# Optimization experiments

Measured on AMD Instinct MI355X. Metric: run time of the kernel, lower is better.

The kernel has to match this reference:

```python
import jax, jax.numpy as jnp
import numpy as np

B, N, F, K = 512, 512, 512, 10
D = F // 2

def setup_inputs() -> dict:
    key = jax.random.key(0)
    k1, k2, k3 = jax.random.split(key, 3)
    ins_emb = jax.random.normal(k1, (B, N, F), dtype=jnp.float32)
    attn = jax.random.uniform(k2, (B, N, 1), dtype=jnp.float32)
    # xavier_uniform for a (D, D) linear weight
    limit = float(np.sqrt(6.0 / (D + D)))
    W = jax.random.uniform(k3, (D, D), dtype=jnp.float32, minval=-limit, maxval=limit)
    return {"ins_emb": ins_emb, "attn": attn, "W": W}

def reference(ins_emb, attn, W):
    d = ins_emb.shape[-1] // 2
    drug = ins_emb[:, :, :d]          # [B, N, d]
    dis = ins_emb[:, :, d:]           # [B, N, d]
    # torch Linear: drug @ W^T, then per-instance dot with dis -> scalar
    proj = jnp.einsum('bnd,ed->bne', drug, W)          # [B, N, d]
    pred = jnp.sum(proj * dis, axis=-1, keepdims=True) # [B, N, 1]
    attn_pred = attn * pred                            # [B, N, 1]
    topk_vals, _ = jax.lax.top_k(attn_pred[:, :, 0], K)  # [B, K]
    return jnp.mean(topk_vals, axis=1, keepdims=True)    # [B, 1]
```

## Files before the change

### kernel.cpp

```cpp
#include <hip/hip_runtime.h>
#include <hip/hip_bf16.h>
#include <cstdint>

#define BB 512
#define NN 512
#define FF 512
#define DD 256
#define KTOP 10
#define BN (BB*NN)
#define BM 32
#define NTILES (BN/BM)
#define GRID 256
#define TPB (NTILES/GRID)

typedef __attribute__((ext_vector_type(8))) short bf16x8;
typedef __attribute__((ext_vector_type(4))) short s16x4;
typedef __attribute__((ext_vector_type(4))) float f32x4;

__device__ __forceinline__ ushort f2bf(float x){
  union { __hip_bfloat16 h; ushort u; } cv;
  cv.h = __float2bfloat16(x);
  return cv.u;
}

__device__ __forceinline__ bf16x8 cvt8(f32x4 a, f32x4 b){
  bf16x8 r;
  r[0]=(short)f2bf(a[0]); r[1]=(short)f2bf(a[1]); r[2]=(short)f2bf(a[2]); r[3]=(short)f2bf(a[3]);
  r[4]=(short)f2bf(b[0]); r[5]=(short)f2bf(b[1]); r[6]=(short)f2bf(b[2]); r[7]=(short)f2bf(b[3]);
  return r;
}

#define GL2LDS(GSRC, LDST)                                                          \
  __builtin_amdgcn_global_load_lds(                                                 \
      (const __attribute__((address_space(1))) uint32_t*)(uintptr_t)(GSRC),         \
      (__attribute__((address_space(3))) uint32_t*)(uint32_t)(uintptr_t)(LDST),     \
      16, 0, 0)

__global__ void wconv(const float* __restrict__ W, ushort* __restrict__ Wbf){
  int i = (blockIdx.x*256 + threadIdx.x)*4;
  float4 v = *reinterpret_cast<const float4*>(W + i);
  s16x4 o;
  o[0] = (short)f2bf(v.x); o[1] = (short)f2bf(v.y);
  o[2] = (short)f2bf(v.z); o[3] = (short)f2bf(v.w);
  *reinterpret_cast<s16x4*>(Wbf + i) = o;
}

__global__ __launch_bounds__(512, 2)
void score_kernel(const float* __restrict__ emb, const float* __restrict__ attn,
                  const ushort* __restrict__ Wbf, float* __restrict__ scores){
  __shared__ float Lbuf[2][BM*FF];
  __shared__ float red[2][8][BM];
  __shared__ float attn_l[TPB*BM];

  const int tid  = threadIdx.x;
  const int w    = tid >> 6;
  const int lane = tid & 63;
  const int g    = lane >> 4;
  const int c    = lane & 15;
  const int s    = w & 3;
  const int h    = w >> 2;

  attn_l[tid]       = attn[blockIdx.x*(TPB*BM) + tid];
  attn_l[tid + 512] = attn[blockIdx.x*(TPB*BM) + 512 + tid];

  bf16x8 Wf[4][4];
#pragma unroll
  for (int eb = 0; eb < 4; ++eb)
#pragma unroll
    for (int kb = 0; kb < 4; ++kb){
      int e = s*64 + eb*16 + c;
      int k = h*128 + kb*32 + g*8;
      Wf[eb][kb] = *reinterpret_cast<const bf16x8*>(Wbf + e*DD + k);
    }

  int offs[8];
#pragma unroll
  for (int i = 0; i < 8; ++i){
    int idx = w*8 + i;
    int r = idx >> 1, hf = idx & 1;
    offs[i] = r*FF + hf*256 + ((lane ^ (r & 7)) << 2);
  }
  const float* tbase = emb + (size_t)blockIdx.x * TPB * (BM*FF);

#pragma unroll
  for (int i = 0; i < 8; ++i)
    GL2LDS(tbase + offs[i], &Lbuf[0][(w*8 + i)*256]);
  __syncthreads();

  int cur = 0;
  for (int t = 0; t < TPB; ++t){
    if (t + 1 < TPB){
      const float* nb = tbase + (size_t)(t+1) * (BM*FF);
#pragma unroll
      for (int i = 0; i < 8; ++i)
        GL2LDS(nb + offs[i], &Lbuf[cur ^ 1][(w*8 + i)*256]);
    }

    const f32x4* Lv = (const f32x4*)&Lbuf[cur][0];
#pragma unroll
    for (int mb = 0; mb < 2; ++mb){
      const int m0 = mb*16;
      const int rb = (m0 + c)*128;
      const int x  = c & 7;
      bf16x8 af[4];
#pragma unroll
      for (int kb = 0; kb < 4; ++kb){
        int ch0 = h*32 + kb*8 + g*2;
        f32x4 q0 = Lv[rb + ((ch0    ) ^ x)];
        f32x4 q1 = Lv[rb + ((ch0 + 1) ^ x)];
        af[kb] = cvt8(q0, q1);
      }
      float rs0=0.f, rs1=0.f, rs2=0.f, rs3=0.f;
#pragma unroll
      for (int eb = 0; eb < 4; ++eb){
        f32x4 acc = {0.f, 0.f, 0.f, 0.f};
#pragma unroll
        for (int kb = 0; kb < 4; ++kb)
          acc = __builtin_amdgcn_mfma_f32_16x16x32_bf16(af[kb], Wf[eb][kb], acc, 0, 0, 0);
        const int sb = 64 + s*16 + eb*4 + (c >> 2);
        const int e3 = c & 3;
#pragma unroll
        for (int j = 0; j < 4; ++j){
          const int row = m0 + g*4 + j;
          const int fi  = row*FF + ((sb ^ (row & 7)) << 2) + e3;
          float d = Lbuf[cur][fi];
          if      (j == 0) rs0 += acc[0]*d;
          else if (j == 1) rs1 += acc[1]*d;
          else if (j == 2) rs2 += acc[2]*d;
          else             rs3 += acc[3]*d;
        }
      }
      rs0 += __shfl_xor(rs0,1); rs0 += __shfl_xor(rs0,2); rs0 += __shfl_xor(rs0,4); rs0 += __shfl_xor(rs0,8);
      rs1 += __shfl_xor(rs1,1); rs1 += __shfl_xor(rs1,2); rs1 += __shfl_xor(rs1,4); rs1 += __shfl_xor(rs1,8);
      rs2 += __shfl_xor(rs2,1); rs2 += __shfl_xor(rs2,2); rs2 += __shfl_xor(rs2,4); rs2 += __shfl_xor(rs2,8);
      rs3 += __shfl_xor(rs3,1); rs3 += __shfl_xor(rs3,2); rs3 += __shfl_xor(rs3,4); rs3 += __shfl_xor(rs3,8);
      if (c == 0){
        red[cur][w][m0 + g*4 + 0] = rs0;
        red[cur][w][m0 + g*4 + 1] = rs1;
        red[cur][w][m0 + g*4 + 2] = rs2;
        red[cur][w][m0 + g*4 + 3] = rs3;
      }
    }

    __syncthreads();

    if (tid < BM){
      float sum = red[cur][0][tid] + red[cur][1][tid] + red[cur][2][tid] + red[cur][3][tid]
                + red[cur][4][tid] + red[cur][5][tid] + red[cur][6][tid] + red[cur][7][tid];
      int row = (blockIdx.x*TPB + t)*BM + tid;
      scores[row] = attn_l[t*BM + tid] * sum;
    }
    cur ^= 1;
  }
}

__global__ void topk_kernel(const float* __restrict__ scores, float* __restrict__ out){
  const int b = blockIdx.x;
  const int lane = threadIdx.x;
  float v0,v1,v2,v3,v4,v5,v6,v7;
  const float* sc = scores + b*NN;
  v0=sc[lane]; v1=sc[64+lane]; v2=sc[128+lane]; v3=sc[192+lane];
  v4=sc[256+lane]; v5=sc[320+lane]; v6=sc[384+lane]; v7=sc[448+lane];
  float total = 0.f;
  for (int it = 0; it < KTOP; ++it){
    float m = v0; int mj = 0;
    if (v1>m){m=v1;mj=1;} if (v2>m){m=v2;mj=2;} if (v3>m){m=v3;mj=3;}
    if (v4>m){m=v4;mj=4;} if (v5>m){m=v5;mj=5;} if (v6>m){m=v6;mj=6;}
    if (v7>m){m=v7;mj=7;}
    float bm = m; int bl = lane;
#pragma unroll
    for (int off = 32; off; off >>= 1){
      float om = __shfl_xor(bm, off);
      int   ol = __shfl_xor(bl, off);
      if (om > bm || (om == bm && ol < bl)){ bm = om; bl = ol; }
    }
    total += bm;
    if (lane == bl){
      if (mj==0) v0=-3.0e38f; else if (mj==1) v1=-3.0e38f;
      else if (mj==2) v2=-3.0e38f; else if (mj==3) v3=-3.0e38f;
      else if (mj==4) v4=-3.0e38f; else if (mj==5) v5=-3.0e38f;
      else if (mj==6) v6=-3.0e38f; else v7=-3.0e38f;
    }
  }
  if (lane == 0) out[b] = total * (1.0f / KTOP);
}

extern "C" void kernel_launch(void* const* d_in, const int* in_sizes, int n_in,
                              void* d_out, int out_size, void* d_ws, size_t ws_size,
                              hipStream_t stream){
  const float* emb  = (const float*)d_in[0];
  const float* attn = (const float*)d_in[1];
  const float* W    = (const float*)d_in[2];
  float* out = (float*)d_out;

  ushort* Wbf    = (ushort*)d_ws;
  float*  scores = (float*)((char*)d_ws + DD*DD*sizeof(ushort));

  wconv<<<64, 256, 0, stream>>>(W, Wbf);
  score_kernel<<<GRID, 512, 0, stream>>>(emb, attn, Wbf, scores);
  topk_kernel<<<BB, 64, 0, stream>>>(scores, out);
}
```

Baseline: 110.0 us.

## Deepen LDS prefetch to three in-flight tiles with smaller row tiles

Halves the row tile from 32 to 16 and uses four LDS buffers instead of two, so three future tiles are prefetched with global_load_lds while the current one is computed. Readiness is tracked with explicit vmcnt waits and a raw s_barrier instead of __syncthreads. The cross-wave reduction and score write for each tile move into the next iteration, which leaves one barrier per tile. The aim is to keep more memory traffic in flight in this bandwidth-bound stream over the embeddings. The cost is more per-tile loop overhead and hand-tuned waitcnt logic that depends on exact load counts.

```diff
diff --git a/kernel.cpp b/kernel.cpp
--- a/kernel.cpp
+++ b/kernel.cpp
@@ -8,7 +8,7 @@
 #define DD 256
 #define KTOP 10
 #define BN (BB*NN)
-#define BM 32
+#define BM 16
 #define NTILES (BN/BM)
 #define GRID 256
 #define TPB (NTILES/GRID)
@@ -48,7 +48,7 @@
 __global__ __launch_bounds__(512, 2)
 void score_kernel(const float* __restrict__ emb, const float* __restrict__ attn,
                   const ushort* __restrict__ Wbf, float* __restrict__ scores){
-  __shared__ float Lbuf[2][BM*FF];
+  __shared__ float Lbuf[4][BM*FF];
   __shared__ float red[2][8][BM];
   __shared__ float attn_l[TPB*BM];
 
@@ -73,84 +73,96 @@
       Wf[eb][kb] = *reinterpret_cast<const bf16x8*>(Wbf + e*DD + k);
     }
 
-  int offs[8];
-#pragma unroll
-  for (int i = 0; i < 8; ++i){
-    int idx = w*8 + i;
+  int offs[4];
+#pragma unroll
+  for (int i = 0; i < 4; ++i){
+    int idx = w*4 + i;
     int r = idx >> 1, hf = idx & 1;
     offs[i] = r*FF + hf*256 + ((lane ^ (r & 7)) << 2);
   }
   const float* tbase = emb + (size_t)blockIdx.x * TPB * (BM*FF);
 
 #pragma unroll
-  for (int i = 0; i < 8; ++i)
-    GL2LDS(tbase + offs[i], &Lbuf[0][(w*8 + i)*256]);
-  __syncthreads();
-
-  int cur = 0;
+  for (int tt = 0; tt < 3; ++tt){
+    const float* nb = tbase + (size_t)tt * (BM*FF);
+#pragma unroll
+    for (int i = 0; i < 4; ++i)
+      GL2LDS(nb + offs[i], &Lbuf[tt][(w*4 + i)*256]);
+  }
+
   for (int t = 0; t < TPB; ++t){
-    if (t + 1 < TPB){
-      const float* nb = tbase + (size_t)(t+1) * (BM*FF);
-#pragma unroll
-      for (int i = 0; i < 8; ++i)
-        GL2LDS(nb + offs[i], &Lbuf[cur ^ 1][(w*8 + i)*256]);
-    }
-
-    const f32x4* Lv = (const f32x4*)&Lbuf[cur][0];
-#pragma unroll
-    for (int mb = 0; mb < 2; ++mb){
-      const int m0 = mb*16;
-      const int rb = (m0 + c)*128;
-      const int x  = c & 7;
-      bf16x8 af[4];
-#pragma unroll
-      for (int kb = 0; kb < 4; ++kb){
-        int ch0 = h*32 + kb*8 + g*2;
-        f32x4 q0 = Lv[rb + ((ch0    ) ^ x)];
-        f32x4 q1 = Lv[rb + ((ch0 + 1) ^ x)];
-        af[kb] = cvt8(q0, q1);
+    if (t + 2 < TPB)      asm volatile("s_waitcnt vmcnt(8) lgkmcnt(0)" ::: "memory");
+    else if (t + 1 < TPB) asm volatile("s_waitcnt vmcnt(4) lgkmcnt(0)" ::: "memory");
+    else                  asm volatile("s_waitcnt vmcnt(0) lgkmcnt(0)" ::: "memory");
+    __builtin_amdgcn_s_barrier();
+    __builtin_amdgcn_sched_barrier(0);
+
+    if (t + 3 < TPB){
+      const float* nb = tbase + (size_t)(t+3) * (BM*FF);
+#pragma unroll
+      for (int i = 0; i < 4; ++i)
+        GL2LDS(nb + offs[i], &Lbuf[(t+3) & 3][(w*4 + i)*256]);
+    }
+
+    if (t > 0 && tid < BM){
+      const int tp = t - 1;
+      float sum = red[tp&1][0][tid] + red[tp&1][1][tid] + red[tp&1][2][tid] + red[tp&1][3][tid]
+                + red[tp&1][4][tid] + red[tp&1][5][tid] + red[tp&1][6][tid] + red[tp&1][7][tid];
+      int row = (blockIdx.x*TPB + tp)*BM + tid;
+      scores[row] = attn_l[tp*BM + tid] * sum;
+    }
+
+    const f32x4* Lv = (const f32x4*)&Lbuf[t & 3][0];
+    const int rb = c*128;
+    const int x  = c & 7;
+    bf16x8 af[4];
+#pragma unroll
+    for (int kb = 0; kb < 4; ++kb){
+      int ch0 = h*32 + kb*8 + g*2;
+      f32x4 q0 = Lv[rb + ((ch0    ) ^ x)];
+      f32x4 q1 = Lv[rb + ((ch0 + 1) ^ x)];
+      af[kb] = cvt8(q0, q1);
+    }
+    float rs0=0.f, rs1=0.f, rs2=0.f, rs3=0.f;
+#pragma unroll
+    for (int eb = 0; eb < 4; ++eb){
+      f32x4 acc = {0.f, 0.f, 0.f, 0.f};
+#pragma unroll
+      for (int kb = 0; kb < 4; ++kb)
+        acc = __builtin_amdgcn_mfma_f32_16x16x32_bf16(af[kb], Wf[eb][kb], acc, 0, 0, 0);
+      const int sb = 64 + s*16 + eb*4 + (c >> 2);
+      const int e3 = c & 3;
+#pragma unroll
+      for (int j = 0; j < 4; ++j){
+        const int row = g*4 + j;
+        const int fi  = row*FF + ((sb ^ (row & 7)) << 2) + e3;
+        float d = Lbuf[t & 3][fi];
+        if      (j == 0) rs0 += acc[0]*d;
+        else if (j == 1) rs1 += acc[1]*d;
+        else if (j == 2) rs2 += acc[2]*d;
+        else             rs3 += acc[3]*d;
       }
-      float rs0=0.f, rs1=0.f, rs2=0.f, rs3=0.f;
-#pragma unroll
-      for (int eb = 0; eb < 4; ++eb){
-        f32x4 acc = {0.f, 0.f, 0.f, 0.f};
-#pragma unroll
-        for (int kb = 0; kb < 4; ++kb)
-          acc = __builtin_amdgcn_mfma_f32_16x16x32_bf16(af[kb], Wf[eb][kb], acc, 0, 0, 0);
-        const int sb = 64 + s*16 + eb*4 + (c >> 2);
-        const int e3 = c & 3;
-#pragma unroll
-        for (int j = 0; j < 4; ++j){
-          const int row = m0 + g*4 + j;
-          const int fi  = row*FF + ((sb ^ (row & 7)) << 2) + e3;
-          float d = Lbuf[cur][fi];
-          if      (j == 0) rs0 += acc[0]*d;
-          else if (j == 1) rs1 += acc[1]*d;
-          else if (j == 2) rs2 += acc[2]*d;
-          else             rs3 += acc[3]*d;
-        }
-      }
-      rs0 += __shfl_xor(rs0,1); rs0 += __shfl_xor(rs0,2); rs0 += __shfl_xor(rs0,4); rs0 += __shfl_xor(rs0,8);
-      rs1 += __shfl_xor(rs1,1); rs1 += __shfl_xor(rs1,2); rs1 += __shfl_xor(rs1,4); rs1 += __shfl_xor(rs1,8);
-      rs2 += __shfl_xor(rs2,1); rs2 += __shfl_xor(rs2,2); rs2 += __shfl_xor(rs2,4); rs2 += __shfl_xor(rs2,8);
-      rs3 += __shfl_xor(rs3,1); rs3 += __shfl_xor(rs3,2); rs3 += __shfl_xor(rs3,4); rs3 += __shfl_xor(rs3,8);
-      if (c == 0){
-        red[cur][w][m0 + g*4 + 0] = rs0;
-        red[cur][w][m0 + g*4 + 1] = rs1;
-        red[cur][w][m0 + g*4 + 2] = rs2;
-        red[cur][w][m0 + g*4 + 3] = rs3;
-      }
-    }
-
-    __syncthreads();
-
-    if (tid < BM){
-      float sum = red[cur][0][tid] + red[cur][1][tid] + red[cur][2][tid] + red[cur][3][tid]
-                + red[cur][4][tid] + red[cur][5][tid] + red[cur][6][tid] + red[cur][7][tid];
-      int row = (blockIdx.x*TPB + t)*BM + tid;
-      scores[row] = attn_l[t*BM + tid] * sum;
-    }
-    cur ^= 1;
+    }
+    rs0 += __shfl_xor(rs0,1); rs0 += __shfl_xor(rs0,2); rs0 += __shfl_xor(rs0,4); rs0 += __shfl_xor(rs0,8);
+    rs1 += __shfl_xor(rs1,1); rs1 += __shfl_xor(rs1,2); rs1 += __shfl_xor(rs1,4); rs1 += __shfl_xor(rs1,8);
+    rs2 += __shfl_xor(rs2,1); rs2 += __shfl_xor(rs2,2); rs2 += __shfl_xor(rs2,4); rs2 += __shfl_xor(rs2,8);
+    rs3 += __shfl_xor(rs3,1); rs3 += __shfl_xor(rs3,2); rs3 += __shfl_xor(rs3,4); rs3 += __shfl_xor(rs3,8);
+    if (c == 0){
+      red[t&1][w][g*4 + 0] = rs0;
+      red[t&1][w][g*4 + 1] = rs1;
+      red[t&1][w][g*4 + 2] = rs2;
+      red[t&1][w][g*4 + 3] = rs3;
+    }
+  }
+
+  asm volatile("s_waitcnt lgkmcnt(0)" ::: "memory");
+  __builtin_amdgcn_s_barrier();
+  if (tid < BM){
+    const int tp = TPB - 1;
+    float sum = red[tp&1][0][tid] + red[tp&1][1][tid] + red[tp&1][2][tid] + red[tp&1][3][tid]
+              + red[tp&1][4][tid] + red[tp&1][5][tid] + red[tp&1][6][tid] + red[tp&1][7][tid];
+    int row = (blockIdx.x*TPB + tp)*BM + tid;
+    scores[row] = attn_l[tp*BM + tid] * sum;
   }
 }
 
```

Result: slower. 116.0 us (+5.5%).

## Fuse weight conversion, scoring and top-k into a single kernel

Applied to the files above, without the earlier changes.

Replaces the three launches (W to bf16 conversion, score kernel, top-k kernel) with one kernel. Each block loads and converts its W fragments from fp32 directly, keeps its 1024 scores (two batches) in shared memory, and runs the top-k selection with two waves at the end. It also issues the first tile's global-to-LDS load before the W loads, so that load overlaps them. This removes two launches and the global round trip of the scores array. In exchange every block repeats the W conversion and reads fp32 W, which doubles W traffic per block.

```diff
diff --git a/kernel.cpp b/kernel.cpp
--- a/kernel.cpp
+++ b/kernel.cpp
@@ -7,14 +7,11 @@
 #define FF 512
 #define DD 256
 #define KTOP 10
-#define BN (BB*NN)
 #define BM 32
-#define NTILES (BN/BM)
 #define GRID 256
-#define TPB (NTILES/GRID)
+#define TPB 32
 
 typedef __attribute__((ext_vector_type(8))) short bf16x8;
-typedef __attribute__((ext_vector_type(4))) short s16x4;
 typedef __attribute__((ext_vector_type(4))) float f32x4;
 
 __device__ __forceinline__ ushort f2bf(float x){
@@ -36,21 +33,13 @@
       (__attribute__((address_space(3))) uint32_t*)(uint32_t)(uintptr_t)(LDST),     \
       16, 0, 0)
 
-__global__ void wconv(const float* __restrict__ W, ushort* __restrict__ Wbf){
-  int i = (blockIdx.x*256 + threadIdx.x)*4;
-  float4 v = *reinterpret_cast<const float4*>(W + i);
-  s16x4 o;
-  o[0] = (short)f2bf(v.x); o[1] = (short)f2bf(v.y);
-  o[2] = (short)f2bf(v.z); o[3] = (short)f2bf(v.w);
-  *reinterpret_cast<s16x4*>(Wbf + i) = o;
-}
-
 __global__ __launch_bounds__(512, 2)
-void score_kernel(const float* __restrict__ emb, const float* __restrict__ attn,
-                  const ushort* __restrict__ Wbf, float* __restrict__ scores){
+void fused_kernel(const float* __restrict__ emb, const float* __restrict__ attn,
+                  const float* __restrict__ W, float* __restrict__ out){
   __shared__ float Lbuf[2][BM*FF];
   __shared__ float red[2][8][BM];
   __shared__ float attn_l[TPB*BM];
+  __shared__ float scores_l[TPB*BM];
 
   const int tid  = threadIdx.x;
   const int w    = tid >> 6;
@@ -60,6 +49,19 @@
   const int s    = w & 3;
   const int h    = w >> 2;
 
+  int offs[8];
+#pragma unroll
+  for (int i = 0; i < 8; ++i){
+    int idx = w*8 + i;
+    int r = idx >> 1, hf = idx & 1;
+    offs[i] = r*FF + hf*256 + ((lane ^ (r & 7)) << 2);
+  }
+  const float* tbase = emb + (size_t)blockIdx.x * (TPB*BM*FF);
+
+#pragma unroll
+  for (int i = 0; i < 8; ++i)
+    GL2LDS(tbase + offs[i], &Lbuf[0][(w*8 + i)*256]);
+
   attn_l[tid]       = attn[blockIdx.x*(TPB*BM) + tid];
   attn_l[tid + 512] = attn[blockIdx.x*(TPB*BM) + 512 + tid];
 
@@ -68,23 +70,12 @@
   for (int eb = 0; eb < 4; ++eb)
 #pragma unroll
     for (int kb = 0; kb < 4; ++kb){
-      int e = s*64 + eb*16 + c;
-      int k = h*128 + kb*32 + g*8;
-      Wf[eb][kb] = *reinterpret_cast<const bf16x8*>(Wbf + e*DD + k);
+      const float* wp = W + (s*64 + eb*16 + c)*DD + h*128 + kb*32 + g*8;
+      f32x4 q0 = *reinterpret_cast<const f32x4*>(wp);
+      f32x4 q1 = *reinterpret_cast<const f32x4*>(wp + 4);
+      Wf[eb][kb] = cvt8(q0, q1);
     }
 
-  int offs[8];
-#pragma unroll
-  for (int i = 0; i < 8; ++i){
-    int idx = w*8 + i;
-    int r = idx >> 1, hf = idx & 1;
-    offs[i] = r*FF + hf*256 + ((lane ^ (r & 7)) << 2);
-  }
-  const float* tbase = emb + (size_t)blockIdx.x * TPB * (BM*FF);
-
-#pragma unroll
-  for (int i = 0; i < 8; ++i)
-    GL2LDS(tbase + offs[i], &Lbuf[0][(w*8 + i)*256]);
   __syncthreads();
 
   int cur = 0;
@@ -147,42 +138,41 @@
     if (tid < BM){
       float sum = red[cur][0][tid] + red[cur][1][tid] + red[cur][2][tid] + red[cur][3][tid]
                 + red[cur][4][tid] + red[cur][5][tid] + red[cur][6][tid] + red[cur][7][tid];
-      int row = (blockIdx.x*TPB + t)*BM + tid;
-      scores[row] = attn_l[t*BM + tid] * sum;
+      scores_l[t*BM + tid] = attn_l[t*BM + tid] * sum;
     }
     cur ^= 1;
   }
-}
 
-__global__ void topk_kernel(const float* __restrict__ scores, float* __restrict__ out){
-  const int b = blockIdx.x;
-  const int lane = threadIdx.x;
-  float v0,v1,v2,v3,v4,v5,v6,v7;
-  const float* sc = scores + b*NN;
-  v0=sc[lane]; v1=sc[64+lane]; v2=sc[128+lane]; v3=sc[192+lane];
-  v4=sc[256+lane]; v5=sc[320+lane]; v6=sc[384+lane]; v7=sc[448+lane];
-  float total = 0.f;
-  for (int it = 0; it < KTOP; ++it){
-    float m = v0; int mj = 0;
-    if (v1>m){m=v1;mj=1;} if (v2>m){m=v2;mj=2;} if (v3>m){m=v3;mj=3;}
-    if (v4>m){m=v4;mj=4;} if (v5>m){m=v5;mj=5;} if (v6>m){m=v6;mj=6;}
-    if (v7>m){m=v7;mj=7;}
-    float bm = m; int bl = lane;
+  __syncthreads();
+
+  if (w < 2){
+    const float* sc = scores_l + w*NN;
+    float v0,v1,v2,v3,v4,v5,v6,v7;
+    v0=sc[lane];     v1=sc[64+lane];  v2=sc[128+lane]; v3=sc[192+lane];
+    v4=sc[256+lane]; v5=sc[320+lane]; v6=sc[384+lane]; v7=sc[448+lane];
+    float total = 0.f;
+    for (int it = 0; it < KTOP; ++it){
+      float m = v0; int mj = 0;
+      if (v1>m){m=v1;mj=1;} if (v2>m){m=v2;mj=2;} if (v3>m){m=v3;mj=3;}
+      if (v4>m){m=v4;mj=4;} if (v5>m){m=v5;mj=5;} if (v6>m){m=v6;mj=6;}
+      if (v7>m){m=v7;mj=7;}
+      float bm = m; int bl = lane;
 #pragma unroll
-    for (int off = 32; off; off >>= 1){
-      float om = __shfl_xor(bm, off);
-      int   ol = __shfl_xor(bl, off);
-      if (om > bm || (om == bm && ol < bl)){ bm = om; bl = ol; }
+      for (int off = 32; off; off >>= 1){
+        float om = __shfl_xor(bm, off);
+        int   ol = __shfl_xor(bl, off);
+        if (om > bm || (om == bm && ol < bl)){ bm = om; bl = ol; }
+      }
+      total += bm;
+      if (lane == bl){
+        if (mj==0) v0=-3.0e38f; else if (mj==1) v1=-3.0e38f;
+        else if (mj==2) v2=-3.0e38f; else if (mj==3) v3=-3.0e38f;
+        else if (mj==4) v4=-3.0e38f; else if (mj==5) v5=-3.0e38f;
+        else if (mj==6) v6=-3.0e38f; else v7=-3.0e38f;
+      }
     }
-    total += bm;
-    if (lane == bl){
-      if (mj==0) v0=-3.0e38f; else if (mj==1) v1=-3.0e38f;
-      else if (mj==2) v2=-3.0e38f; else if (mj==3) v3=-3.0e38f;
-      else if (mj==4) v4=-3.0e38f; else if (mj==5) v5=-3.0e38f;
-      else if (mj==6) v6=-3.0e38f; else v7=-3.0e38f;
-    }
+    if (lane == 0) out[blockIdx.x*2 + w] = total * (1.0f / KTOP);
   }
-  if (lane == 0) out[b] = total * (1.0f / KTOP);
 }
 
 extern "C" void kernel_launch(void* const* d_in, const int* in_sizes, int n_in,
@@ -193,10 +183,5 @@
   const float* W    = (const float*)d_in[2];
   float* out = (float*)d_out;
 
-  ushort* Wbf    = (ushort*)d_ws;
-  float*  scores = (float*)((char*)d_ws + DD*DD*sizeof(ushort));
-
-  wconv<<<64, 256, 0, stream>>>(W, Wbf);
-  score_kernel<<<GRID, 512, 0, stream>>>(emb, attn, Wbf, scores);
-  topk_kernel<<<BB, 64, 0, stream>>>(scores, out);
+  fused_kernel<<<GRID, 512, 0, stream>>>(emb, attn, W, out);
 }
```

Result: no change. 108.0 us (-1.8%).
